# Kernel optimization log

Hardware: AMD Instinct MI355X
Metric: run time of the kernel (lower is better)

Reference implementation:

```python
import jax, jax.numpy as jnp
import numpy as np


def gather_neighbour(pc, neighbor_idx):
    # pc: [B, N, d], neighbor_idx: [B, M, K] -> [B, M, K, d]
    return jax.vmap(lambda p, i: p[i])(pc, neighbor_idx)


def relative_pos_encoding(xyz, neigh_idx):
    # xyz: [B, N, 3], neigh_idx: [B, N, K]
    neighbor_xyz = gather_neighbour(xyz, neigh_idx)                 # [B, N, K, 3]
    xyz_tile = jnp.broadcast_to(xyz[:, :, None, :], neighbor_xyz.shape)
    relative_xyz = xyz_tile - neighbor_xyz
    relative_dis = jnp.sqrt(jnp.sum(relative_xyz * relative_xyz, axis=-1, keepdims=True))
    return jnp.concatenate([relative_dis, relative_xyz, xyz_tile, neighbor_xyz], axis=-1)  # [B,N,K,10]


def random_sample(feature, pool_idx):
    # feature: [B, d, N, 1], pool_idx: [B, Np, K] -> [B, d, Np, 1]
    feat = feature[..., 0]                                          # [B, d, N]
    B, Np, K = pool_idx.shape
    d = feat.shape[1]
    g = jnp.take_along_axis(feat, pool_idx.reshape(B, 1, Np * K), axis=2)
    g = g.reshape(B, d, Np, K)
    return jnp.max(g, axis=3, keepdims=True)


def nearest_interpolation(feature, interp_idx):
    # feature: [B, d, Np, 1], interp_idx: [B, U, 1] -> [B, d, U, 1]
    feat = feature[..., 0]                                          # [B, d, Np]
    B, U = interp_idx.shape[0], interp_idx.shape[1]
    g = jnp.take_along_axis(feat, interp_idx.reshape(B, 1, U), axis=2)
    return g[..., None]


def setup_inputs() -> dict:
    key = jax.random.key(0)
    k = jax.random.split(key, 6)
    B, N, K, d = 4, 65536, 16, 32
    Np = N // 4
    # neighbor indices that never point to self (avoids sqrt(0) NaN in bwd)
    base = jnp.arange(N, dtype=jnp.int32)[None, :, None]
    off = jax.random.randint(k[1], (B, N, K), 1, N, dtype=jnp.int32)
    neigh_idx = (base + off) % N
    return {
        "xyz": jax.random.normal(k[0], (B, N, 3), jnp.float32),
        "neigh_idx": neigh_idx,
        "feat_pool": jax.random.normal(k[2], (B, d, N, 1), jnp.float32),
        "pool_idx": jax.random.randint(k[3], (B, Np, K), 0, N, dtype=jnp.int32),
        "feat_interp": jax.random.normal(k[4], (B, d, Np, 1), jnp.float32),
        "interp_idx": jax.random.randint(k[5], (B, N, 1), 0, Np, dtype=jnp.int32),
    }


def reference(xyz, neigh_idx, feat_pool, pool_idx, feat_interp, interp_idx):
    rel = relative_pos_encoding(xyz, neigh_idx)        # [B, N, K, 10]
    pooled = random_sample(feat_pool, pool_idx)        # [B, d, Np, 1]
    interp = nearest_interpolation(feat_interp, interp_idx)  # [B, d, N, 1]
    return rel, pooled, interp
```

## Files before the change

### kernel.cpp

```cpp
#include <hip/hip_runtime.h>
#include <math.h>

#define BATCH 4
#define NPTS  65536
#define KNBR  16
#define DF    32
#define NPOOL 16384

typedef float f32x4 __attribute__((ext_vector_type(4)));

#define FTP_ELEMS   ((size_t)BATCH * NPTS * DF)
#define FTI_ELEMS   ((size_t)BATCH * NPOOL * DF)
#define XYZ4_ELEMS  ((size_t)BATCH * NPTS * 4)

#define T1_BLKS (BATCH * (NPTS / 32))
#define T2_BLKS (BATCH * (NPOOL / 32))
#define T3_BLKS ((BATCH * NPTS) / 256)
__global__ __launch_bounds__(256) void prep_kernel(
    const float* __restrict__ feat_pool, const float* __restrict__ feat_interp,
    const float* __restrict__ xyz,
    float* __restrict__ ftp, float* __restrict__ fti, float* __restrict__ xyz4)
{
    __shared__ float tile[32][33];
    const int bid = blockIdx.x;
    const int t = threadIdx.x;
    if (bid < T1_BLKS + T2_BLKS) {
        const float* in; float* outp; int nn, tb;
        if (bid < T1_BLKS) { in = feat_pool;  outp = ftp; nn = NPTS;  tb = bid; }
        else               { in = feat_interp; outp = fti; nn = NPOOL; tb = bid - T1_BLKS; }
        const int tpb = nn >> 5;
        const int b  = tb / tpb;
        const int n0 = (tb % tpb) << 5;
        const int nl = t & 31;
        const int dl = t >> 5;
        #pragma unroll
        for (int it = 0; it < 4; ++it) {
            const int d = dl + it * 8;
            tile[d][nl] = __builtin_nontemporal_load(&in[(size_t)(b * DF + d) * nn + n0 + nl]);
        }
        __syncthreads();
        #pragma unroll
        for (int it = 0; it < 4; ++it) {
            const int n = dl + it * 8;
            outp[((size_t)b * nn + n0 + n) * DF + nl] = tile[nl][n];
        }
    } else {
        const int p = (bid - T1_BLKS - T2_BLKS) * 256 + t;
        const float x = __builtin_nontemporal_load(&xyz[(size_t)p * 3 + 0]);
        const float y = __builtin_nontemporal_load(&xyz[(size_t)p * 3 + 1]);
        const float z = __builtin_nontemporal_load(&xyz[(size_t)p * 3 + 2]);
        f32x4 v = { x, y, z, 0.f };
        ((f32x4*)xyz4)[p] = v;
    }
}

#define R_BLKS 16384
#define P_BLKS 1024
#define I_BLKS 4096
#define MAIN_BLKS (R_BLKS + P_BLKS + I_BLKS)

__global__ __launch_bounds__(256) void fused_main(
    const float* __restrict__ xyz4, const int* __restrict__ nidx,
    const float* __restrict__ ftp,  const int* __restrict__ pidx,
    const float* __restrict__ fti,  const int* __restrict__ iidx,
    float* __restrict__ rel, float* __restrict__ pooled, float* __restrict__ interp)
{
    __shared__ char smem[12800];
    const int g = blockIdx.x / 21;
    const int m = blockIdx.x % 21;
    const int t = threadIdx.x;

    if (m < 16) {
        float* s = (float*)smem;
        const int rblk = g * 16 + m;
        const int e = rblk * 256 + t;
        const int b = e >> 20;
        const int n = (e >> 4) & (NPTS - 1);
        const int j = __builtin_nontemporal_load(&nidx[e]);
        const float4 c = ((const float4*)xyz4)[b * NPTS + n];
        const float4 q = ((const float4*)xyz4)[b * NPTS + j];
        const float rx = c.x - q.x, ry = c.y - q.y, rz = c.z - q.z;
        const float dist = sqrtf(rx * rx + ry * ry + rz * rz);
        float* st = s + t * 10;
        st[0] = dist; st[1] = rx;  st[2] = ry;  st[3] = rz;
        st[4] = c.x;  st[5] = c.y; st[6] = c.z;
        st[7] = q.x;  st[8] = q.y; st[9] = q.z;
        __syncthreads();
        f32x4* o4 = (f32x4*)(rel + (size_t)rblk * 2560);
        const f32x4* s4 = (const f32x4*)smem;
        __builtin_nontemporal_store(s4[t],       &o4[t]);
        __builtin_nontemporal_store(s4[t + 256], &o4[t + 256]);
        if (t < 128) __builtin_nontemporal_store(s4[t + 512], &o4[t + 512]);
    } else if (m == 16) {
        int*   s_idx = (int*)smem;
        float* s_out = (float*)(smem + 4096);
        const int bpb = NPOOL / 64;
        const int b   = g / bpb;
        const int np0 = (g % bpb) * 64;
        ((int4*)s_idx)[t] = ((const int4*)(pidx + (size_t)(b * NPOOL + np0) * KNBR))[t];
        __syncthreads();
        const float4* fb4 = (const float4*)(ftp + (size_t)b * NPTS * DF);
        const int l8 = t & 7;
        #pragma unroll
        for (int it = 0; it < 2; ++it) {
            const int u = (t >> 3) + it * 32;
            float4 acc = make_float4(-INFINITY, -INFINITY, -INFINITY, -INFINITY);
            #pragma unroll
            for (int k = 0; k < KNBR; ++k) {
                const int idx = s_idx[u * KNBR + k];
                const float4 v = fb4[(size_t)idx * 8 + l8];
                acc.x = fmaxf(acc.x, v.x); acc.y = fmaxf(acc.y, v.y);
                acc.z = fmaxf(acc.z, v.z); acc.w = fmaxf(acc.w, v.w);
            }
            float* so = s_out + u * 33 + l8 * 4;
            so[0] = acc.x; so[1] = acc.y; so[2] = acc.z; so[3] = acc.w;
        }
        __syncthreads();
        #pragma unroll
        for (int w = 0; w < 8; ++w) {
            const int flat = w * 256 + t;
            const int u  = flat & 63;
            const int dd = flat >> 6;
            __builtin_nontemporal_store(s_out[u * 33 + dd],
                &pooled[(size_t)(b * DF + dd) * NPOOL + np0 + u]);
        }
    } else {
        int*   s_idx = (int*)smem;
        float* s_out = (float*)(smem + 256);
        const int i   = g * 4 + (m - 17);
        const int bpb = NPTS / 64;
        const int b   = i / bpb;
        const int u0  = (i % bpb) * 64;
        if (t < 64) s_idx[t] = iidx[b * NPTS + u0 + t];
        __syncthreads();
        const float4* fb4 = (const float4*)(fti + (size_t)b * NPOOL * DF);
        const int l8 = t & 7;
        #pragma unroll
        for (int it = 0; it < 2; ++it) {
            const int u = (t >> 3) + it * 32;
            const int idx = s_idx[u];
            const float4 v = fb4[(size_t)idx * 8 + l8];
            float* so = s_out + u * 33 + l8 * 4;
            so[0] = v.x; so[1] = v.y; so[2] = v.z; so[3] = v.w;
        }
        __syncthreads();
        #pragma unroll
        for (int w = 0; w < 8; ++w) {
            const int flat = w * 256 + t;
            const int u  = flat & 63;
            const int dd = flat >> 6;
            __builtin_nontemporal_store(s_out[u * 33 + dd],
                &interp[(size_t)(b * DF + dd) * NPTS + u0 + u]);
        }
    }
}

__global__ __launch_bounds__(256) void relpos_kernel(
    const float* __restrict__ xyz, const int* __restrict__ nidx,
    float* __restrict__ out)
{
    __shared__ float s[2560];
    const int tid = threadIdx.x;
    const int e = blockIdx.x * 256 + tid;
    const int b = e >> 20;
    const int n = (e >> 4) & (NPTS - 1);
    const int j = nidx[e];
    const float* c = xyz + (size_t)(b * NPTS + n) * 3;
    const float* g = xyz + (size_t)(b * NPTS + j) * 3;
    const float cx = c[0], cy = c[1], cz = c[2];
    const float nx = g[0], ny = g[1], nz = g[2];
    const float rx = cx - nx, ry = cy - ny, rz = cz - nz;
    const float dist = sqrtf(rx * rx + ry * ry + rz * rz);
    float* st = s + tid * 10;
    st[0] = dist; st[1] = rx; st[2] = ry; st[3] = rz;
    st[4] = cx;   st[5] = cy; st[6] = cz;
    st[7] = nx;   st[8] = ny; st[9] = nz;
    __syncthreads();
    float4* o4 = (float4*)(out + (size_t)blockIdx.x * 2560);
    const float4* s4 = (const float4*)s;
    o4[tid]       = s4[tid];
    o4[tid + 256] = s4[tid + 256];
    if (tid < 128) o4[tid + 512] = s4[tid + 512];
}

__global__ __launch_bounds__(256) void pool_kernel_naive(
    const float* __restrict__ feat, const int* __restrict__ pidx,
    float* __restrict__ out)
{
    const int i  = blockIdx.x * 256 + threadIdx.x;
    const int np = i & (NPOOL - 1);
    const int bd = i >> 14;
    const int b  = bd >> 5;
    const int4* ip = (const int4*)(pidx + (size_t)(b * NPOOL + np) * KNBR);
    const float* f = feat + (size_t)bd * NPTS;
    float m = -INFINITY;
    #pragma unroll
    for (int q = 0; q < 4; ++q) {
        const int4 v = ip[q];
        m = fmaxf(m, f[v.x]); m = fmaxf(m, f[v.y]);
        m = fmaxf(m, f[v.z]); m = fmaxf(m, f[v.w]);
    }
    out[i] = m;
}

__global__ __launch_bounds__(256) void interp_kernel_naive(
    const float* __restrict__ feat, const int* __restrict__ iidx,
    float* __restrict__ out)
{
    const int i  = blockIdx.x * 256 + threadIdx.x;
    const int u  = i & (NPTS - 1);
    const int bd = i >> 16;
    const int b  = bd >> 5;
    out[i] = feat[(size_t)bd * NPOOL + iidx[b * NPTS + u]];
}

extern "C" void kernel_launch(void* const* d_in, const int* in_sizes, int n_in,
                              void* d_out, int out_size, void* d_ws, size_t ws_size,
                              hipStream_t stream) {
    const float* xyz         = (const float*)d_in[0];
    const int*   neigh_idx   = (const int*)d_in[1];
    const float* feat_pool   = (const float*)d_in[2];
    const int*   pool_idx    = (const int*)d_in[3];
    const float* feat_interp = (const float*)d_in[4];
    const int*   interp_idx  = (const int*)d_in[5];

    float* out    = (float*)d_out;
    float* rel    = out;
    float* pooled = rel + (size_t)BATCH * NPTS * KNBR * 10;
    float* interp = pooled + (size_t)BATCH * DF * NPOOL;

    const size_t need = (FTP_ELEMS + FTI_ELEMS + XYZ4_ELEMS) * sizeof(float);
    if (ws_size >= need) {
        float* ftp  = (float*)d_ws;
        float* fti  = ftp + FTP_ELEMS;
        float* xyz4 = fti + FTI_ELEMS;
        prep_kernel<<<T1_BLKS + T2_BLKS + T3_BLKS, 256, 0, stream>>>(
            feat_pool, feat_interp, xyz, ftp, fti, xyz4);
        fused_main<<<MAIN_BLKS, 256, 0, stream>>>(
            xyz4, neigh_idx, ftp, pool_idx, fti, interp_idx, rel, pooled, interp);
    } else {
        relpos_kernel<<<(BATCH * NPTS * KNBR) / 256, 256, 0, stream>>>(xyz, neigh_idx, rel);
        pool_kernel_naive<<<(BATCH * DF * NPOOL) / 256, 256, 0, stream>>>(feat_pool, pool_idx, pooled);
        interp_kernel_naive<<<(BATCH * DF * NPTS) / 256, 256, 0, stream>>>(feat_interp, interp_idx, interp);
    }
}
```

Before: 312.2 us.

## Rebalance kernels: fuse relpos with feature transposes, drop xyz4 padding pass

Moves the relative-position work out of the gather kernel and into the transpose/prep kernel. The streaming relpos writes now overlap with the feature transposes, and the second kernel holds only the pool and interp gathers. The padded xyz4 buffer is removed, so relpos reads the raw xyz with three scalar loads, trading an extra pass and workspace for unaligned gather loads. The pool and interp outputs are now written as 128-bit vector stores instead of scalar stores.

New measurement: 308.8 us. Within noise of the previous version (-1.1%).

```diff
diff --git a/kernel.cpp b/kernel.cpp
--- a/kernel.cpp
+++ b/kernel.cpp
@@ -11,23 +11,33 @@
 
 #define FTP_ELEMS   ((size_t)BATCH * NPTS * DF)
 #define FTI_ELEMS   ((size_t)BATCH * NPOOL * DF)
-#define XYZ4_ELEMS  ((size_t)BATCH * NPTS * 4)
 
 #define T1_BLKS (BATCH * (NPTS / 32))
 #define T2_BLKS (BATCH * (NPOOL / 32))
-#define T3_BLKS ((BATCH * NPTS) / 256)
-__global__ __launch_bounds__(256) void prep_kernel(
+#define R_BLKS  ((BATCH * NPTS * KNBR) / 256)
+#define A_GROUPS 2048
+#define A_BLKS  (A_GROUPS * 13)
+
+#define P_BLKS 1024
+#define I_BLKS 4096
+#define B_BLKS (P_BLKS + I_BLKS)
+
+__global__ __launch_bounds__(256) void streamA_kernel(
+    const float* __restrict__ xyz, const int* __restrict__ nidx,
     const float* __restrict__ feat_pool, const float* __restrict__ feat_interp,
-    const float* __restrict__ xyz,
-    float* __restrict__ ftp, float* __restrict__ fti, float* __restrict__ xyz4)
-{
-    __shared__ float tile[32][33];
-    const int bid = blockIdx.x;
+    float* __restrict__ ftp, float* __restrict__ fti, float* __restrict__ rel)
+{
+    __shared__ float smem[2560];
+    const int g = blockIdx.x / 13;
+    const int m = blockIdx.x % 13;
     const int t = threadIdx.x;
-    if (bid < T1_BLKS + T2_BLKS) {
-        const float* in; float* outp; int nn, tb;
-        if (bid < T1_BLKS) { in = feat_pool;  outp = ftp; nn = NPTS;  tb = bid; }
-        else               { in = feat_interp; outp = fti; nn = NPOOL; tb = bid - T1_BLKS; }
+
+    if (m < 5) {
+        float (*tile)[33] = (float(*)[33])smem;
+        int tb = g * 5 + m;
+        const float* in; float* outp; int nn;
+        if (tb < T1_BLKS) { in = feat_pool;   outp = ftp; nn = NPTS; }
+        else              { in = feat_interp; outp = fti; nn = NPOOL; tb -= T1_BLKS; }
         const int tpb = nn >> 5;
         const int b  = tb / tpb;
         const int n0 = (tb % tpb) << 5;
@@ -45,53 +55,41 @@
             outp[((size_t)b * nn + n0 + n) * DF + nl] = tile[nl][n];
         }
     } else {
-        const int p = (bid - T1_BLKS - T2_BLKS) * 256 + t;
-        const float x = __builtin_nontemporal_load(&xyz[(size_t)p * 3 + 0]);
-        const float y = __builtin_nontemporal_load(&xyz[(size_t)p * 3 + 1]);
-        const float z = __builtin_nontemporal_load(&xyz[(size_t)p * 3 + 2]);
-        f32x4 v = { x, y, z, 0.f };
-        ((f32x4*)xyz4)[p] = v;
-    }
-}
-
-#define R_BLKS 16384
-#define P_BLKS 1024
-#define I_BLKS 4096
-#define MAIN_BLKS (R_BLKS + P_BLKS + I_BLKS)
-
-__global__ __launch_bounds__(256) void fused_main(
-    const float* __restrict__ xyz4, const int* __restrict__ nidx,
-    const float* __restrict__ ftp,  const int* __restrict__ pidx,
-    const float* __restrict__ fti,  const int* __restrict__ iidx,
-    float* __restrict__ rel, float* __restrict__ pooled, float* __restrict__ interp)
-{
-    __shared__ char smem[12800];
-    const int g = blockIdx.x / 21;
-    const int m = blockIdx.x % 21;
-    const int t = threadIdx.x;
-
-    if (m < 16) {
-        float* s = (float*)smem;
-        const int rblk = g * 16 + m;
+        const int rblk = g * 8 + (m - 5);
         const int e = rblk * 256 + t;
         const int b = e >> 20;
         const int n = (e >> 4) & (NPTS - 1);
         const int j = __builtin_nontemporal_load(&nidx[e]);
-        const float4 c = ((const float4*)xyz4)[b * NPTS + n];
-        const float4 q = ((const float4*)xyz4)[b * NPTS + j];
-        const float rx = c.x - q.x, ry = c.y - q.y, rz = c.z - q.z;
+        const float* cp = xyz + (size_t)(b * NPTS + n) * 3;
+        const float* qp = xyz + (size_t)(b * NPTS + j) * 3;
+        const float cx = cp[0], cy = cp[1], cz = cp[2];
+        const float qx = qp[0], qy = qp[1], qz = qp[2];
+        const float rx = cx - qx, ry = cy - qy, rz = cz - qz;
         const float dist = sqrtf(rx * rx + ry * ry + rz * rz);
-        float* st = s + t * 10;
-        st[0] = dist; st[1] = rx;  st[2] = ry;  st[3] = rz;
-        st[4] = c.x;  st[5] = c.y; st[6] = c.z;
-        st[7] = q.x;  st[8] = q.y; st[9] = q.z;
+        float* st = smem + t * 10;
+        st[0] = dist; st[1] = rx; st[2] = ry; st[3] = rz;
+        st[4] = cx;   st[5] = cy; st[6] = cz;
+        st[7] = qx;   st[8] = qy; st[9] = qz;
         __syncthreads();
         f32x4* o4 = (f32x4*)(rel + (size_t)rblk * 2560);
         const f32x4* s4 = (const f32x4*)smem;
         __builtin_nontemporal_store(s4[t],       &o4[t]);
         __builtin_nontemporal_store(s4[t + 256], &o4[t + 256]);
         if (t < 128) __builtin_nontemporal_store(s4[t + 512], &o4[t + 512]);
-    } else if (m == 16) {
+    }
+}
+
+__global__ __launch_bounds__(256) void gatherB_kernel(
+    const float* __restrict__ ftp, const int* __restrict__ pidx,
+    const float* __restrict__ fti, const int* __restrict__ iidx,
+    float* __restrict__ pooled, float* __restrict__ interp)
+{
+    __shared__ char smem[12544];
+    const int g = blockIdx.x / 5;
+    const int m = blockIdx.x % 5;
+    const int t = threadIdx.x;
+
+    if (m == 0) {
         int*   s_idx = (int*)smem;
         float* s_out = (float*)(smem + 4096);
         const int bpb = NPOOL / 64;
@@ -117,17 +115,19 @@
         }
         __syncthreads();
         #pragma unroll
-        for (int w = 0; w < 8; ++w) {
-            const int flat = w * 256 + t;
-            const int u  = flat & 63;
-            const int dd = flat >> 6;
-            __builtin_nontemporal_store(s_out[u * 33 + dd],
-                &pooled[(size_t)(b * DF + dd) * NPOOL + np0 + u]);
+        for (int it = 0; it < 2; ++it) {
+            const int flat = it * 256 + t;
+            const int dd = flat >> 4;
+            const int u  = (flat & 15) * 4;
+            f32x4 v = { s_out[(u + 0) * 33 + dd], s_out[(u + 1) * 33 + dd],
+                        s_out[(u + 2) * 33 + dd], s_out[(u + 3) * 33 + dd] };
+            __builtin_nontemporal_store(v,
+                (f32x4*)&pooled[(size_t)(b * DF + dd) * NPOOL + np0 + u]);
         }
     } else {
         int*   s_idx = (int*)smem;
         float* s_out = (float*)(smem + 256);
-        const int i   = g * 4 + (m - 17);
+        const int i   = g * 4 + (m - 1);
         const int bpb = NPTS / 64;
         const int b   = i / bpb;
         const int u0  = (i % bpb) * 64;
@@ -145,12 +145,14 @@
         }
         __syncthreads();
         #pragma unroll
-        for (int w = 0; w < 8; ++w) {
-            const int flat = w * 256 + t;
-            const int u  = flat & 63;
-            const int dd = flat >> 6;
-            __builtin_nontemporal_store(s_out[u * 33 + dd],
-                &interp[(size_t)(b * DF + dd) * NPTS + u0 + u]);
+        for (int it = 0; it < 2; ++it) {
+            const int flat = it * 256 + t;
+            const int dd = flat >> 4;
+            const int u  = (flat & 15) * 4;
+            f32x4 v = { s_out[(u + 0) * 33 + dd], s_out[(u + 1) * 33 + dd],
+                        s_out[(u + 2) * 33 + dd], s_out[(u + 3) * 33 + dd] };
+            __builtin_nontemporal_store(v,
+                (f32x4*)&interp[(size_t)(b * DF + dd) * NPTS + u0 + u]);
         }
     }
 }
@@ -229,17 +231,16 @@
     float* pooled = rel + (size_t)BATCH * NPTS * KNBR * 10;
     float* interp = pooled + (size_t)BATCH * DF * NPOOL;
 
-    const size_t need = (FTP_ELEMS + FTI_ELEMS + XYZ4_ELEMS) * sizeof(float);
+    const size_t need = (FTP_ELEMS + FTI_ELEMS) * sizeof(float);
     if (ws_size >= need) {
-        float* ftp  = (float*)d_ws;
-        float* fti  = ftp + FTP_ELEMS;
-        float* xyz4 = fti + FTI_ELEMS;
-        prep_kernel<<<T1_BLKS + T2_BLKS + T3_BLKS, 256, 0, stream>>>(
-            feat_pool, feat_interp, xyz, ftp, fti, xyz4);
-        fused_main<<<MAIN_BLKS, 256, 0, stream>>>(
-            xyz4, neigh_idx, ftp, pool_idx, fti, interp_idx, rel, pooled, interp);
+        float* ftp = (float*)d_ws;
+        float* fti = ftp + FTP_ELEMS;
+        streamA_kernel<<<A_BLKS, 256, 0, stream>>>(
+            xyz, neigh_idx, feat_pool, feat_interp, ftp, fti, rel);
+        gatherB_kernel<<<B_BLKS, 256, 0, stream>>>(
+            ftp, pool_idx, fti, interp_idx, pooled, interp);
     } else {
-        relpos_kernel<<<(BATCH * NPTS * KNBR) / 256, 256, 0, stream>>>(xyz, neigh_idx, rel);
+        relpos_kernel<<<R_BLKS, 256, 0, stream>>>(xyz, neigh_idx, rel);
         pool_kernel_naive<<<(BATCH * DF * NPOOL) / 256, 256, 0, stream>>>(feat_pool, pool_idx, pooled);
         interp_kernel_naive<<<(BATCH * DF * NPTS) / 256, 256, 0, stream>>>(feat_interp, interp_idx, interp);
     }
```
